# Kernel optimization log

Measured on AMD Instinct MI355X. Metric: run time of the kernel, lower is better.

The kernel has to match this reference:

```python
import jax, jax.numpy as jnp
import numpy as np

H, L, NB = 128, 2048, 64  # features, seq len, half state size (conj-symmetric N=128)


def _forward(u, x_re, x_im, Lambda_re, Lambda_im, B_re, B_im, C_re, C_im, D, d):
    Lam = (Lambda_re + 1j * Lambda_im).astype(jnp.complex64)   # (H, NB) discrete diag A
    B = (B_re + 1j * B_im).astype(jnp.complex64)               # (H, NB)
    C = (C_re + 1j * C_im).astype(jnp.complex64)               # (H, NB)
    x0 = (x_re + 1j * x_im).astype(jnp.complex64)              # (H, NB) initial state
    Hn, Ln = u.shape
    # scan elements (A_t, b_t, d_t); identity element (1, x0, False) prepended at t=0
    A = jnp.concatenate([jnp.ones((Hn, 1, NB), jnp.complex64),
                         jnp.broadcast_to(Lam[:, None, :], (Hn, Ln, NB))], axis=1)
    b = jnp.concatenate([x0[:, None, :],
                         B[:, None, :] * u[:, :, None].astype(jnp.complex64)], axis=1)
    dd = jnp.concatenate([jnp.zeros((1,), bool), d.astype(bool)])[None, :, None]  # (1, L+1, 1)

    def combine(lhs, rhs):
        # reset-aware associative combine: if right done-flag set, drop left contribution
        A_i, b_i, c_i = lhs
        A_j, b_j, c_j = rhs
        return (jnp.where(c_j, A_j, A_j * A_i),
                jnp.where(c_j, b_j, A_j * b_i + b_j),
                jnp.logical_or(c_i, c_j))

    _, xs, _ = jax.lax.associative_scan(combine, (A, b, dd), axis=1)
    xs = xs[:, 1:]                                             # (H, L, NB) hidden states
    # conj symmetry: y_t = 2*Re(C @ x_t) + D * u_t
    y = 2.0 * jnp.real(jnp.einsum('hn,hln->hl', C, xs)) + D[:, None] * u
    return y, xs[:, -1]


def setup_inputs():
    key = jax.random.key(0)
    ks = jax.random.split(key, 8)
    # stable ZOH-discretized HiPPO-like diagonal system (mirrors LSSL-f init)
    dts = jnp.logspace(-3.0, -1.0, H)                          # (H,) per-feature timescales
    k = jnp.arange(NB, dtype=jnp.float32)
    lam_c = -0.5 + 1j * jnp.pi * (2.0 * k + 1.0)               # (NB,) continuous poles
    lam_d = jnp.exp(dts[:, None] * lam_c[None, :]).astype(jnp.complex64)  # (H, NB), |.|<1
    Bc = ((jax.random.normal(ks[0], (NB,)) + 1j * jax.random.normal(ks[1], (NB,)))
          / jnp.sqrt(2.0 * NB)).astype(jnp.complex64)
    Bd = (((lam_d - 1.0) / lam_c[None, :]) * Bc[None, :]).astype(jnp.complex64)  # (H, NB)
    C = ((jax.random.normal(ks[2], (H, NB)) + 1j * jax.random.normal(ks[3], (H, NB)))
         / jnp.sqrt(float(NB))).astype(jnp.complex64)
    return {
        "u": jax.random.normal(ks[4], (H, L), jnp.float32),
        "x_re": jnp.zeros((H, NB), jnp.float32),
        "x_im": jnp.zeros((H, NB), jnp.float32),
        "Lambda_re": jnp.real(lam_d).astype(jnp.float32),
        "Lambda_im": jnp.imag(lam_d).astype(jnp.float32),
        "B_re": jnp.real(Bd).astype(jnp.float32),
        "B_im": jnp.imag(Bd).astype(jnp.float32),
        "C_re": jnp.real(C).astype(jnp.float32),
        "C_im": jnp.imag(C).astype(jnp.float32),
        "D": jax.random.normal(ks[5], (H,), jnp.float32),
        "d": jax.random.bernoulli(ks[6], 0.01, (L,)),
    }


def reference(u, x_re, x_im, Lambda_re, Lambda_im, B_re, B_im, C_re, C_im, D, d):
    return _forward(u, x_re, x_im, Lambda_re, Lambda_im, B_re, B_im, C_re, C_im, D, d)
```

## Files before the change

kernel.cpp:

```cpp
#include <hip/hip_runtime.h>

#define Hn 128
#define Ln 2048
#define NBn 64
#define K 64
#define G 32
#define PITCH 68


__global__ __launch_bounds__(64) void phase1_local(
    const float* __restrict__ u,
    const float* __restrict__ Lre,  const float* __restrict__ Lim,
    const float* __restrict__ Bre,  const float* __restrict__ Bim,
    const float* __restrict__ Cre,  const float* __restrict__ Cim,
    const float* __restrict__ Dv,   const int* __restrict__ dflag,
    float* __restrict__ out,
    float4* __restrict__ Sum)
{
    __shared__ float g_s[K * PITCH];
    __shared__ float u_s[K];

    const int g = blockIdx.x, h = blockIdx.y, n = threadIdx.x;
    const int hn = h * NBn + n;
    const int l0 = g * K;

    const float lre = Lre[hn], lim = Lim[hn];
    const float bre = Bre[hn], bim = Bim[hn];
    const float c2re =  2.0f * Cre[hn];
    const float c2im = -2.0f * Cim[hn];
    const float Dh   = Dv[h];

    u_s[n] = u[h * Ln + l0 + n];
    const int dn = dflag[l0 + n];
    const unsigned long long m = __ballot(dn != 0);
    __syncthreads();

    float zre = 0.f, zim = 0.f;
    #pragma unroll
    for (int k = 0; k < K; ++k) {
        const bool  rs  = (m >> k) & 1ull;
        const float ul  = u_s[k];
        const float lrk = rs ? 0.f : lre;
        const float lik = rs ? 0.f : lim;
        const float bur = bre * ul;
        const float bui = bim * ul;
        const float nr = fmaf(lrk, zre, fmaf(-lik, zim, bur));
        const float ni = fmaf(lrk, zim, fmaf( lik, zre, bui));
        zre = nr; zim = ni;
        g_s[k * PITCH + n] = fmaf(c2re, zre, c2im * zim);
    }
    __syncthreads();

    const float4* row4 = reinterpret_cast<const float4*>(g_s + n * PITCH);
    float a0 = 0.f, a1 = 0.f, a2 = 0.f, a3 = 0.f;
    #pragma unroll
    for (int k = 0; k < NBn / 4; ++k) {
        const float4 v = row4[k];
        a0 += v.x; a1 += v.y; a2 += v.z; a3 += v.w;
    }
    out[h * Ln + l0 + n] = (a0 + a1) + (a2 + a3) + Dh * u_s[n];

    float pr = lre, pi = lim;
    #pragma unroll
    for (int it = 0; it < 6; ++it) {
        const float sr2 = pr * pr - pi * pi;
        const float si2 = 2.f * pr * pi;
        pr = sr2; pi = si2;
    }
    if (m) { pr = 0.f; pi = 0.f; }
    Sum[(h * G + g) * NBn + n] = make_float4(pr, pi, zre, zim);
}

__global__ __launch_bounds__(64) void phase2_combine(
    const float* __restrict__ x_re, const float* __restrict__ x_im,
    const float4* __restrict__ Sum,
    float2* __restrict__ Sin,
    float* __restrict__ out)
{
    const int h = blockIdx.x, n = threadIdx.x;
    const int hn = h * NBn + n;
    float sre = x_re[hn], sim = x_im[hn];
    #pragma unroll
    for (int g = 0; g < G; ++g) {
        const int idx = (h * G + g) * NBn + n;
        const float4 s = Sum[idx];
        Sin[idx] = make_float2(sre, sim);
        const float nr = fmaf(s.x, sre, fmaf(-s.y, sim, s.z));
        const float ni = fmaf(s.x, sim, fmaf( s.y, sre, s.w));
        sre = nr; sim = ni;
    }
    float* xlast = out + Hn * Ln;
    xlast[2 * hn + 0] = sre;
    xlast[2 * hn + 1] = sim;
}

__global__ __launch_bounds__(64) void phase3_fixup(
    const float* __restrict__ Lre, const float* __restrict__ Lim,
    const float* __restrict__ Cre, const float* __restrict__ Cim,
    const int* __restrict__ dflag,
    const float2* __restrict__ Sin,
    float* __restrict__ out)
{
    __shared__ float g_s[K * PITCH];

    const int g = blockIdx.x, h = blockIdx.y, n = threadIdx.x;
    const int hn = h * NBn + n;
    const int l0 = g * K;
    const int idx = (h * G + g) * NBn + n;

    const float2 s = Sin[idx];
    const float cr = Cre[hn],  ci = Cim[hn];
    const float lre = Lre[hn], lim = Lim[hn];

    const int dn = dflag[l0 + n];
    const unsigned long long bal = __ballot(dn != 0);
    const int kr = bal ? (__ffsll(bal) - 1) : K;

    const float pr = cr * s.x - ci * s.y;
    const float pi = cr * s.y + ci * s.x;
    const float l2r = lre * lre - lim * lim;
    const float l2i = 2.f * lre * lim;

    float tAr = fmaf(lre, pr, -lim * pi);
    float tAi = fmaf(lre, pi,  lim * pr);
    float tBr = fmaf(l2r, pr, -l2i * pi);
    float tBi = fmaf(l2r, pi,  l2i * pr);
    g_s[0 * PITCH + n] = tAr;
    g_s[1 * PITCH + n] = tBr;
    #pragma unroll
    for (int k = 2; k < K; k += 2) {
        const float nAr = fmaf(l2r, tAr, -l2i * tAi);
        const float nAi = fmaf(l2r, tAi,  l2i * tAr);
        tAr = nAr; tAi = nAi;
        g_s[k * PITCH + n] = tAr;
        const float nBr = fmaf(l2r, tBr, -l2i * tBi);
        const float nBi = fmaf(l2r, tBi,  l2i * tBr);
        tBr = nBr; tBi = nBi;
        g_s[(k + 1) * PITCH + n] = tBr;
    }
    __syncthreads();

    const float4* row4 = reinterpret_cast<const float4*>(g_s + n * PITCH);
    float a0 = 0.f, a1 = 0.f, a2 = 0.f, a3 = 0.f;
    #pragma unroll
    for (int k = 0; k < NBn / 4; ++k) {
        const float4 v = row4[k];
        a0 += v.x; a1 += v.y; a2 += v.z; a3 += v.w;
    }
    if (n < kr)
        out[h * Ln + l0 + n] += 2.f * ((a0 + a1) + (a2 + a3));
}

extern "C" void kernel_launch(void* const* d_in, const int* in_sizes, int n_in,
                              void* d_out, int out_size, void* d_ws, size_t ws_size,
                              hipStream_t stream) {
    const float* u    = (const float*)d_in[0];
    const float* x_re = (const float*)d_in[1];
    const float* x_im = (const float*)d_in[2];
    const float* Lre  = (const float*)d_in[3];
    const float* Lim  = (const float*)d_in[4];
    const float* Bre  = (const float*)d_in[5];
    const float* Bim  = (const float*)d_in[6];
    const float* Cre  = (const float*)d_in[7];
    const float* Cim  = (const float*)d_in[8];
    const float* Dv   = (const float*)d_in[9];
    const int*   dfl  = (const int*)d_in[10];
    float* out = (float*)d_out;

    const int HGN = Hn * G * NBn;
    float4* Sum = (float4*)d_ws;
    float2* Sin = (float2*)(Sum + HGN);

    dim3 grid(G, Hn);
    phase1_local<<<grid, 64, 0, stream>>>(u, Lre, Lim, Bre, Bim, Cre, Cim,
                                          Dv, dfl, out, Sum);
    phase2_combine<<<Hn, 64, 0, stream>>>(x_re, x_im, Sum, Sin, out);
    phase3_fixup<<<grid, 64, 0, stream>>>(Lre, Lim, Cre, Cim, dfl, Sin, out);
}
```

Measured before the change: 93.25 us.

## Fuse three-phase chunked scan into one kernel per feature with shared-memory carry

Replaces the three kernel launches (local chunk scan, sequential carry combine, fixup) with one kernel per feature row. Eight waves each own four chunks, and chunk-end states and reset flags pass through shared memory instead of global workspace. The state is pre-multiplied by 2C to save work, with a division recovering the final state, and a no-reset fast path is added. This removes launch overhead and global round-trips at the cost of only 128 blocks and a serial per-wave chunk loop. The final-state division by |2C|^2 also risks precision loss when C is small.

```diff
diff --git a/kernel.cpp b/kernel.cpp
--- a/kernel.cpp
+++ b/kernel.cpp
@@ -5,150 +5,157 @@
 #define NBn 64
 #define K 64
 #define G 32
+#define W 8
+#define CPW 4
 #define PITCH 68
 
-
-__global__ __launch_bounds__(64) void phase1_local(
+__global__ __launch_bounds__(512) void ssm_fused(
     const float* __restrict__ u,
+    const float* __restrict__ x_re, const float* __restrict__ x_im,
     const float* __restrict__ Lre,  const float* __restrict__ Lim,
     const float* __restrict__ Bre,  const float* __restrict__ Bim,
     const float* __restrict__ Cre,  const float* __restrict__ Cim,
     const float* __restrict__ Dv,   const int* __restrict__ dflag,
-    float* __restrict__ out,
-    float4* __restrict__ Sum)
+    float* __restrict__ out)
 {
-    __shared__ float g_s[K * PITCH];
-    __shared__ float u_s[K];
+    __shared__ float  g_s[W][K * PITCH];
+    __shared__ float2 b_s[G][NBn];
+    __shared__ int    f_s[G];
 
-    const int g = blockIdx.x, h = blockIdx.y, n = threadIdx.x;
-    const int hn = h * NBn + n;
-    const int l0 = g * K;
+    const int h   = blockIdx.x;
+    const int tid = threadIdx.x;
+    const int w   = tid >> 6;
+    const int n   = tid & 63;
+    const int hn  = h * NBn + n;
 
     const float lre = Lre[hn], lim = Lim[hn];
-    const float bre = Bre[hn], bim = Bim[hn];
-    const float c2re =  2.0f * Cre[hn];
-    const float c2im = -2.0f * Cim[hn];
-    const float Dh   = Dv[h];
+    const float cr  = Cre[hn], ci  = Cim[hn];
+    const float br  = Bre[hn], bi  = Bim[hn];
+    const float Dh  = Dv[h];
+    const float cbr2 = 2.f * (cr * br - ci * bi);
+    const float cbi2 = 2.f * (cr * bi + ci * br);
 
-    u_s[n] = u[h * Ln + l0 + n];
-    const int dn = dflag[l0 + n];
-    const unsigned long long m = __ballot(dn != 0);
-    __syncthreads();
+    float l64r = lre, l64i = lim;
+    #pragma unroll
+    for (int it = 0; it < 6; ++it) {
+        const float a  = l64r * l64r - l64i * l64i;
+        const float b2 = 2.f * l64r * l64i;
+        l64r = a; l64i = b2;
+    }
 
-    float zre = 0.f, zim = 0.f;
+    float ybase[CPW];
+    unsigned long long mask[CPW];
+    float* gbuf = g_s[w];
+
     #pragma unroll
-    for (int k = 0; k < K; ++k) {
-        const bool  rs  = (m >> k) & 1ull;
-        const float ul  = u_s[k];
-        const float lrk = rs ? 0.f : lre;
-        const float lik = rs ? 0.f : lim;
-        const float bur = bre * ul;
-        const float bui = bim * ul;
-        const float nr = fmaf(lrk, zre, fmaf(-lik, zim, bur));
-        const float ni = fmaf(lrk, zim, fmaf( lik, zre, bui));
-        zre = nr; zim = ni;
-        g_s[k * PITCH + n] = fmaf(c2re, zre, c2im * zim);
+    for (int j = 0; j < CPW; ++j) {
+        const int g  = w * CPW + j;
+        const int l0 = g * K;
+        const float ul = u[h * Ln + l0 + n];
+        const int   dn = dflag[l0 + n];
+        const unsigned long long m = __ballot(dn != 0);
+        mask[j] = m;
+        gbuf[64] = 0.f;
+        __shared__ float u_s[W][K];
+        u_s[w][n] = ul;
+
+        float wr = 0.f, wi = 0.f;
+        if (m == 0ull) {
+            #pragma unroll
+            for (int k = 0; k < K; ++k) {
+                const float uk = u_s[w][k];
+                const float nr = fmaf(lre, wr, fmaf(-lim, wi, cbr2 * uk));
+                const float ni = fmaf(lre, wi, fmaf( lim, wr, cbi2 * uk));
+                wr = nr; wi = ni;
+                gbuf[k * PITCH + n] = wr;
+            }
+        } else {
+            #pragma unroll
+            for (int k = 0; k < K; ++k) {
+                const bool  rs  = (m >> k) & 1ull;
+                const float lrk = rs ? 0.f : lre;
+                const float lik = rs ? 0.f : lim;
+                const float uk  = u_s[w][k];
+                const float nr = fmaf(lrk, wr, fmaf(-lik, wi, cbr2 * uk));
+                const float ni = fmaf(lrk, wi, fmaf( lik, wr, cbi2 * uk));
+                wr = nr; wi = ni;
+                gbuf[k * PITCH + n] = wr;
+            }
+        }
+        b_s[g][n] = make_float2(wr, wi);
+        if (n == 0) f_s[g] = (m != 0ull) ? 1 : 0;
+
+        const float4* row4 = reinterpret_cast<const float4*>(gbuf + n * PITCH);
+        float a0 = 0.f, a1 = 0.f, a2 = 0.f, a3 = 0.f;
+        #pragma unroll
+        for (int k2 = 0; k2 < K / 4; ++k2) {
+            const float4 v = row4[k2];
+            a0 += v.x; a1 += v.y; a2 += v.z; a3 += v.w;
+        }
+        ybase[j] = (a0 + a1) + (a2 + a3) + Dh * ul;
     }
     __syncthreads();
 
-    const float4* row4 = reinterpret_cast<const float4*>(g_s + n * PITCH);
-    float a0 = 0.f, a1 = 0.f, a2 = 0.f, a3 = 0.f;
-    #pragma unroll
-    for (int k = 0; k < NBn / 4; ++k) {
-        const float4 v = row4[k];
-        a0 += v.x; a1 += v.y; a2 += v.z; a3 += v.w;
-    }
-    out[h * Ln + l0 + n] = (a0 + a1) + (a2 + a3) + Dh * u_s[n];
-
-    float pr = lre, pi = lim;
-    #pragma unroll
-    for (int it = 0; it < 6; ++it) {
-        const float sr2 = pr * pr - pi * pi;
-        const float si2 = 2.f * pr * pi;
-        pr = sr2; pi = si2;
-    }
-    if (m) { pr = 0.f; pi = 0.f; }
-    Sum[(h * G + g) * NBn + n] = make_float4(pr, pi, zre, zim);
-}
-
-__global__ __launch_bounds__(64) void phase2_combine(
-    const float* __restrict__ x_re, const float* __restrict__ x_im,
-    const float4* __restrict__ Sum,
-    float2* __restrict__ Sin,
-    float* __restrict__ out)
-{
-    const int h = blockIdx.x, n = threadIdx.x;
-    const int hn = h * NBn + n;
-    float sre = x_re[hn], sim = x_im[hn];
+    const float x0r = x_re[hn], x0i = x_im[hn];
+    float sr = 2.f * (cr * x0r - ci * x0i);
+    float si = 2.f * (cr * x0i + ci * x0r);
+    float sinr[CPW], sini[CPW];
     #pragma unroll
     for (int g = 0; g < G; ++g) {
-        const int idx = (h * G + g) * NBn + n;
-        const float4 s = Sum[idx];
-        Sin[idx] = make_float2(sre, sim);
-        const float nr = fmaf(s.x, sre, fmaf(-s.y, sim, s.z));
-        const float ni = fmaf(s.x, sim, fmaf( s.y, sre, s.w));
-        sre = nr; sim = ni;
+        if ((g >> 2) == w) { sinr[g & 3] = sr; sini[g & 3] = si; }
+        const float2 b  = b_s[g][n];
+        const bool  rst = f_s[g] != 0;
+        const float ar  = rst ? 0.f : l64r;
+        const float ai  = rst ? 0.f : l64i;
+        const float nr = fmaf(ar, sr, fmaf(-ai, si, b.x));
+        const float ni = fmaf(ar, si, fmaf( ai, sr, b.y));
+        sr = nr; si = ni;
     }
-    float* xlast = out + Hn * Ln;
-    xlast[2 * hn + 0] = sre;
-    xlast[2 * hn + 1] = sim;
-}
+    if (w == W - 1) {
+        const float c2r = 2.f * cr, c2i = 2.f * ci;
+        const float inv = 1.f / (c2r * c2r + c2i * c2i);
+        float* xlast = out + Hn * Ln;
+        xlast[2 * hn + 0] = (sr * c2r + si * c2i) * inv;
+        xlast[2 * hn + 1] = (si * c2r - sr * c2i) * inv;
+    }
 
-__global__ __launch_bounds__(64) void phase3_fixup(
-    const float* __restrict__ Lre, const float* __restrict__ Lim,
-    const float* __restrict__ Cre, const float* __restrict__ Cim,
-    const int* __restrict__ dflag,
-    const float2* __restrict__ Sin,
-    float* __restrict__ out)
-{
-    __shared__ float g_s[K * PITCH];
-
-    const int g = blockIdx.x, h = blockIdx.y, n = threadIdx.x;
-    const int hn = h * NBn + n;
-    const int l0 = g * K;
-    const int idx = (h * G + g) * NBn + n;
-
-    const float2 s = Sin[idx];
-    const float cr = Cre[hn],  ci = Cim[hn];
-    const float lre = Lre[hn], lim = Lim[hn];
-
-    const int dn = dflag[l0 + n];
-    const unsigned long long bal = __ballot(dn != 0);
-    const int kr = bal ? (__ffsll(bal) - 1) : K;
-
-    const float pr = cr * s.x - ci * s.y;
-    const float pi = cr * s.y + ci * s.x;
     const float l2r = lre * lre - lim * lim;
     const float l2i = 2.f * lre * lim;
+    #pragma unroll
+    for (int j = 0; j < CPW; ++j) {
+        const int g  = w * CPW + j;
+        const int l0 = g * K;
+        const unsigned long long m = mask[j];
+        const int kr = m ? (__ffsll((long long)m) - 1) : K;
 
-    float tAr = fmaf(lre, pr, -lim * pi);
-    float tAi = fmaf(lre, pi,  lim * pr);
-    float tBr = fmaf(l2r, pr, -l2i * pi);
-    float tBi = fmaf(l2r, pi,  l2i * pr);
-    g_s[0 * PITCH + n] = tAr;
-    g_s[1 * PITCH + n] = tBr;
-    #pragma unroll
-    for (int k = 2; k < K; k += 2) {
-        const float nAr = fmaf(l2r, tAr, -l2i * tAi);
-        const float nAi = fmaf(l2r, tAi,  l2i * tAr);
-        tAr = nAr; tAi = nAi;
-        g_s[k * PITCH + n] = tAr;
-        const float nBr = fmaf(l2r, tBr, -l2i * tBi);
-        const float nBi = fmaf(l2r, tBi,  l2i * tBr);
-        tBr = nBr; tBi = nBi;
-        g_s[(k + 1) * PITCH + n] = tBr;
+        const float pr = sinr[j], pi = sini[j];
+        float tAr = fmaf(lre, pr, -lim * pi);
+        float tAi = fmaf(lre, pi,  lim * pr);
+        float tBr = fmaf(l2r, pr, -l2i * pi);
+        float tBi = fmaf(l2r, pi,  l2i * pr);
+        gbuf[0 * PITCH + n] = tAr;
+        gbuf[1 * PITCH + n] = tBr;
+        #pragma unroll
+        for (int k = 2; k < K; k += 2) {
+            const float nAr = fmaf(l2r, tAr, -l2i * tAi);
+            const float nAi = fmaf(l2r, tAi,  l2i * tAr);
+            tAr = nAr; tAi = nAi;
+            gbuf[k * PITCH + n] = tAr;
+            const float nBr = fmaf(l2r, tBr, -l2i * tBi);
+            const float nBi = fmaf(l2r, tBi,  l2i * tBr);
+            tBr = nBr; tBi = nBi;
+            gbuf[(k + 1) * PITCH + n] = tBr;
+        }
+        const float4* row4 = reinterpret_cast<const float4*>(gbuf + n * PITCH);
+        float a0 = 0.f, a1 = 0.f, a2 = 0.f, a3 = 0.f;
+        #pragma unroll
+        for (int k2 = 0; k2 < K / 4; ++k2) {
+            const float4 v = row4[k2];
+            a0 += v.x; a1 += v.y; a2 += v.z; a3 += v.w;
+        }
+        const float corr = (n < kr) ? ((a0 + a1) + (a2 + a3)) : 0.f;
+        out[h * Ln + l0 + n] = ybase[j] + corr;
     }
-    __syncthreads();
-
-    const float4* row4 = reinterpret_cast<const float4*>(g_s + n * PITCH);
-    float a0 = 0.f, a1 = 0.f, a2 = 0.f, a3 = 0.f;
-    #pragma unroll
-    for (int k = 0; k < NBn / 4; ++k) {
-        const float4 v = row4[k];
-        a0 += v.x; a1 += v.y; a2 += v.z; a3 += v.w;
-    }
-    if (n < kr)
-        out[h * Ln + l0 + n] += 2.f * ((a0 + a1) + (a2 + a3));
 }
 
 extern "C" void kernel_launch(void* const* d_in, const int* in_sizes, int n_in,
@@ -167,13 +174,6 @@
     const int*   dfl  = (const int*)d_in[10];
     float* out = (float*)d_out;
 
-    const int HGN = Hn * G * NBn;
-    float4* Sum = (float4*)d_ws;
-    float2* Sin = (float2*)(Sum + HGN);
-
-    dim3 grid(G, Hn);
-    phase1_local<<<grid, 64, 0, stream>>>(u, Lre, Lim, Bre, Bim, Cre, Cim,
-                                          Dv, dfl, out, Sum);
-    phase2_combine<<<Hn, 64, 0, stream>>>(x_re, x_im, Sum, Sin, out);
-    phase3_fixup<<<grid, 64, 0, stream>>>(Lre, Lim, Cre, Cim, dfl, Sin, out);
+    ssm_fused<<<Hn, W * 64, 0, stream>>>(u, x_re, x_im, Lre, Lim,
+                                         Bre, Bim, Cre, Cim, Dv, dfl, out);
 }
```

Measured after the change: 92.09 us. Within noise of the previous version (-1.2%).

## Scan C-scaled state, add reset-free fast path, pad shared rows by one

Applied to the files above, without the earlier changes.

The state is pre-multiplied by 2*C, so the per-step output is just the real part of the scaled state. This removes the per-step C multiply in phase1 and the C rotation in phase3, and phase2 divides 2*C back out for the final state. A branch-free loop handles chunks with no resets, and the shared-memory pitch becomes 65 with scalar reads in place of float4. The risks are a division by |2C|^2, which can lose precision or blow up when C is near zero, and the loss of vectorized LDS reads.

```diff
diff --git a/kernel.cpp b/kernel.cpp
--- a/kernel.cpp
+++ b/kernel.cpp
@@ -5,7 +5,7 @@
 #define NBn 64
 #define K 64
 #define G 32
-#define PITCH 68
+#define PITCH 65
 
 
 __global__ __launch_bounds__(64) void phase1_local(
@@ -25,38 +25,47 @@
     const int l0 = g * K;
 
     const float lre = Lre[hn], lim = Lim[hn];
-    const float bre = Bre[hn], bim = Bim[hn];
-    const float c2re =  2.0f * Cre[hn];
-    const float c2im = -2.0f * Cim[hn];
-    const float Dh   = Dv[h];
+    const float br  = Bre[hn], bi  = Bim[hn];
+    const float cr  = Cre[hn], ci  = Cim[hn];
+    const float Dh  = Dv[h];
+    const float cbr2 = 2.f * (cr * br - ci * bi);
+    const float cbi2 = 2.f * (cr * bi + ci * br);
 
     u_s[n] = u[h * Ln + l0 + n];
-    const int dn = dflag[l0 + n];
-    const unsigned long long m = __ballot(dn != 0);
+    const unsigned long long m = __ballot(dflag[l0 + n] != 0);
     __syncthreads();
 
-    float zre = 0.f, zim = 0.f;
-    #pragma unroll
-    for (int k = 0; k < K; ++k) {
-        const bool  rs  = (m >> k) & 1ull;
-        const float ul  = u_s[k];
-        const float lrk = rs ? 0.f : lre;
-        const float lik = rs ? 0.f : lim;
-        const float bur = bre * ul;
-        const float bui = bim * ul;
-        const float nr = fmaf(lrk, zre, fmaf(-lik, zim, bur));
-        const float ni = fmaf(lrk, zim, fmaf( lik, zre, bui));
-        zre = nr; zim = ni;
-        g_s[k * PITCH + n] = fmaf(c2re, zre, c2im * zim);
+    float wr = 0.f, wi = 0.f;
+    if (m == 0ull) {
+        #pragma unroll
+        for (int k = 0; k < K; ++k) {
+            const float uk = u_s[k];
+            const float nr = fmaf(lre, wr, fmaf(-lim, wi, cbr2 * uk));
+            const float ni = fmaf(lre, wi, fmaf( lim, wr, cbi2 * uk));
+            wr = nr; wi = ni;
+            g_s[k * PITCH + n] = wr;
+        }
+    } else {
+        #pragma unroll
+        for (int k = 0; k < K; ++k) {
+            const bool  rs  = (m >> k) & 1ull;
+            const float lrk = rs ? 0.f : lre;
+            const float lik = rs ? 0.f : lim;
+            const float uk  = u_s[k];
+            const float nr = fmaf(lrk, wr, fmaf(-lik, wi, cbr2 * uk));
+            const float ni = fmaf(lrk, wi, fmaf( lik, wr, cbi2 * uk));
+            wr = nr; wi = ni;
+            g_s[k * PITCH + n] = wr;
+        }
     }
     __syncthreads();
 
-    const float4* row4 = reinterpret_cast<const float4*>(g_s + n * PITCH);
+    const float* row = g_s + n * PITCH;
     float a0 = 0.f, a1 = 0.f, a2 = 0.f, a3 = 0.f;
     #pragma unroll
-    for (int k = 0; k < NBn / 4; ++k) {
-        const float4 v = row4[k];
-        a0 += v.x; a1 += v.y; a2 += v.z; a3 += v.w;
+    for (int k = 0; k < NBn; k += 4) {
+        a0 += row[k + 0]; a1 += row[k + 1];
+        a2 += row[k + 2]; a3 += row[k + 3];
     }
     out[h * Ln + l0 + n] = (a0 + a1) + (a2 + a3) + Dh * u_s[n];
 
@@ -68,18 +77,22 @@
         pr = sr2; pi = si2;
     }
     if (m) { pr = 0.f; pi = 0.f; }
-    Sum[(h * G + g) * NBn + n] = make_float4(pr, pi, zre, zim);
+    Sum[(h * G + g) * NBn + n] = make_float4(pr, pi, wr, wi);
 }
 
 __global__ __launch_bounds__(64) void phase2_combine(
     const float* __restrict__ x_re, const float* __restrict__ x_im,
+    const float* __restrict__ Cre,  const float* __restrict__ Cim,
     const float4* __restrict__ Sum,
     float2* __restrict__ Sin,
     float* __restrict__ out)
 {
     const int h = blockIdx.x, n = threadIdx.x;
     const int hn = h * NBn + n;
-    float sre = x_re[hn], sim = x_im[hn];
+    const float cr = Cre[hn], ci = Cim[hn];
+    const float x0r = x_re[hn], x0i = x_im[hn];
+    float sre = 2.f * (cr * x0r - ci * x0i);
+    float sim = 2.f * (cr * x0i + ci * x0r);
     #pragma unroll
     for (int g = 0; g < G; ++g) {
         const int idx = (h * G + g) * NBn + n;
@@ -89,14 +102,15 @@
         const float ni = fmaf(s.x, sim, fmaf( s.y, sre, s.w));
         sre = nr; sim = ni;
     }
+    const float c2r = 2.f * cr, c2i = 2.f * ci;
+    const float inv = 1.f / (c2r * c2r + c2i * c2i);
     float* xlast = out + Hn * Ln;
-    xlast[2 * hn + 0] = sre;
-    xlast[2 * hn + 1] = sim;
+    xlast[2 * hn + 0] = (sre * c2r + sim * c2i) * inv;
+    xlast[2 * hn + 1] = (sim * c2r - sre * c2i) * inv;
 }
 
 __global__ __launch_bounds__(64) void phase3_fixup(
     const float* __restrict__ Lre, const float* __restrict__ Lim,
-    const float* __restrict__ Cre, const float* __restrict__ Cim,
     const int* __restrict__ dflag,
     const float2* __restrict__ Sin,
     float* __restrict__ out)
@@ -106,25 +120,20 @@
     const int g = blockIdx.x, h = blockIdx.y, n = threadIdx.x;
     const int hn = h * NBn + n;
     const int l0 = g * K;
-    const int idx = (h * G + g) * NBn + n;
 
-    const float2 s = Sin[idx];
-    const float cr = Cre[hn],  ci = Cim[hn];
+    const float2 s = Sin[(h * G + g) * NBn + n];
     const float lre = Lre[hn], lim = Lim[hn];
 
-    const int dn = dflag[l0 + n];
-    const unsigned long long bal = __ballot(dn != 0);
-    const int kr = bal ? (__ffsll(bal) - 1) : K;
+    const unsigned long long bal = __ballot(dflag[l0 + n] != 0);
+    const int kr = bal ? (__ffsll((long long)bal) - 1) : K;
 
-    const float pr = cr * s.x - ci * s.y;
-    const float pi = cr * s.y + ci * s.x;
     const float l2r = lre * lre - lim * lim;
     const float l2i = 2.f * lre * lim;
 
-    float tAr = fmaf(lre, pr, -lim * pi);
-    float tAi = fmaf(lre, pi,  lim * pr);
-    float tBr = fmaf(l2r, pr, -l2i * pi);
-    float tBi = fmaf(l2r, pi,  l2i * pr);
+    float tAr = fmaf(lre, s.x, -lim * s.y);
+    float tAi = fmaf(lre, s.y,  lim * s.x);
+    float tBr = fmaf(l2r, s.x, -l2i * s.y);
+    float tBi = fmaf(l2r, s.y,  l2i * s.x);
     g_s[0 * PITCH + n] = tAr;
     g_s[1 * PITCH + n] = tBr;
     #pragma unroll
@@ -140,15 +149,15 @@
     }
     __syncthreads();
 
-    const float4* row4 = reinterpret_cast<const float4*>(g_s + n * PITCH);
+    const float* row = g_s + n * PITCH;
     float a0 = 0.f, a1 = 0.f, a2 = 0.f, a3 = 0.f;
     #pragma unroll
-    for (int k = 0; k < NBn / 4; ++k) {
-        const float4 v = row4[k];
-        a0 += v.x; a1 += v.y; a2 += v.z; a3 += v.w;
+    for (int k = 0; k < NBn; k += 4) {
+        a0 += row[k + 0]; a1 += row[k + 1];
+        a2 += row[k + 2]; a3 += row[k + 3];
     }
     if (n < kr)
-        out[h * Ln + l0 + n] += 2.f * ((a0 + a1) + (a2 + a3));
+        out[h * Ln + l0 + n] += (a0 + a1) + (a2 + a3);
 }
 
 extern "C" void kernel_launch(void* const* d_in, const int* in_sizes, int n_in,
@@ -174,6 +183,6 @@
     dim3 grid(G, Hn);
     phase1_local<<<grid, 64, 0, stream>>>(u, Lre, Lim, Bre, Bim, Cre, Cim,
                                           Dv, dfl, out, Sum);
-    phase2_combine<<<Hn, 64, 0, stream>>>(x_re, x_im, Sum, Sin, out);
-    phase3_fixup<<<grid, 64, 0, stream>>>(Lre, Lim, Cre, Cim, dfl, Sin, out);
+    phase2_combine<<<Hn, 64, 0, stream>>>(x_re, x_im, Cre, Cim, Sum, Sin, out);
+    phase3_fixup<<<grid, 64, 0, stream>>>(Lre, Lim, dfl, Sin, out);
 }
```

Measured after the change: 88.65 us. 4.9% less time.
